# Optimization experiments

Hardware: AMD Instinct MI355X
Metric: run time of the kernel (lower is better)

The kernel has to match this reference:

```python
import jax, jax.numpy as jnp
import numpy as np

BETA = 30.0


def setup_inputs() -> dict:
    key = jax.random.key(0)
    k_x, k1, k2, k3, kv = jax.random.split(key, 5)
    B, D = 4096, 128
    N = 32  # nodes per hidden layer
    VALUE_SCALE = 500.0
    return {
        "x": jax.random.normal(k_x, (B, D), dtype=jnp.float32),
        "W1": jax.random.normal(k1, (N, D), dtype=jnp.float32),
        "W2": jax.random.normal(k2, (N, D), dtype=jnp.float32),
        "W3": jax.random.normal(k3, (N, D), dtype=jnp.float32),
        "V": jax.random.normal(kv, (1, N, N, N), dtype=jnp.float32) / VALUE_SCALE,
    }


def reference(x, W1, W2, W3, V):
    # feat='sf': every gating layer reads the raw input x (h is never updated).
    # gate_i = sigmoid(beta * x @ W_i^T), shape [B, 32]
    g1 = jax.nn.sigmoid(BETA * (x @ W1.T))
    g2 = jax.nn.sigmoid(BETA * (x @ W2.T))
    g3 = jax.nn.sigmoid(BETA * (x @ W3.T))
    # prod='op': cp[b,i,j,k] = g1[b,i]*g2[b,j]*g3[b,k];
    # out[b] = sum_{ijk} cp[b,i,j,k] * V[0,i,j,k]  -- expressed as one contraction.
    return jnp.einsum("bi,bj,bk,ijk->b", g1, g2, g3, V[0])
```

## Files before the change

kernel.cpp:

```cpp
#include <hip/hip_runtime.h>


#define BETA 30.0f

__device__ __forceinline__ float f4c(const float4 v, int c) {
    return c == 0 ? v.x : (c == 1 ? v.y : (c == 2 ? v.z : v.w));
}

__global__ __launch_bounds__(256, 2) void dlgn_v11_kernel(
    const float* __restrict__ x,
    const float* __restrict__ W1,
    const float* __restrict__ W2,
    const float* __restrict__ W3,
    const float* __restrict__ V,
    float* __restrict__ out)
{
    __shared__ float xlds[8 * 160];
    __shared__ float Gs[8][100];
    __shared__ float red[4][8];

    const int t  = threadIdx.x;
    const int b0 = blockIdx.x * 8;

    {
        const int r    = t >> 5;
        const int col4 = t & 31;
        const float4 xv = ((const float4*)(x + (size_t)(b0 + r) * 128))[col4];
        const int skc = col4 >> 2, sc = col4 & 3;
        *(float4*)&xlds[r * 160 + skc * 20 + sc * 4] = xv;
    }

    const int fl = t >> 3;
    const int kc = t & 7;
    float4 w1c[4], w2c[4], w3c[4];
    {
        const float4* W1r = (const float4*)(W1 + fl * 128 + kc * 16);
        const float4* W2r = (const float4*)(W2 + fl * 128 + kc * 16);
        const float4* W3r = (const float4*)(W3 + fl * 128 + kc * 16);
#pragma unroll
        for (int c = 0; c < 4; ++c) {
            w1c[c] = W1r[c]; w2c[c] = W2r[c]; w3c[c] = W3r[c];
        }
    }
    __syncthreads();

    float acc[3][8];
#pragma unroll
    for (int m = 0; m < 3; ++m)
#pragma unroll
        for (int r = 0; r < 8; ++r) acc[m][r] = 0.f;

#pragma unroll
    for (int r = 0; r < 8; ++r) {
        float4 xc[4];
#pragma unroll
        for (int c = 0; c < 4; ++c)
            xc[c] = *(const float4*)&xlds[r * 160 + kc * 20 + c * 4];
#pragma unroll
        for (int c = 0; c < 4; ++c) {
            acc[0][r] = fmaf(w1c[c].x, xc[c].x, acc[0][r]);
            acc[0][r] = fmaf(w1c[c].y, xc[c].y, acc[0][r]);
            acc[0][r] = fmaf(w1c[c].z, xc[c].z, acc[0][r]);
            acc[0][r] = fmaf(w1c[c].w, xc[c].w, acc[0][r]);
            acc[1][r] = fmaf(w2c[c].x, xc[c].x, acc[1][r]);
            acc[1][r] = fmaf(w2c[c].y, xc[c].y, acc[1][r]);
            acc[1][r] = fmaf(w2c[c].z, xc[c].z, acc[1][r]);
            acc[1][r] = fmaf(w2c[c].w, xc[c].w, acc[1][r]);
            acc[2][r] = fmaf(w3c[c].x, xc[c].x, acc[2][r]);
            acc[2][r] = fmaf(w3c[c].y, xc[c].y, acc[2][r]);
            acc[2][r] = fmaf(w3c[c].z, xc[c].z, acc[2][r]);
            acc[2][r] = fmaf(w3c[c].w, xc[c].w, acc[2][r]);
        }
    }

    const float4* V4 = (const float4*)V;
    float4 v[32];
#pragma unroll
    for (int i = 0; i < 32; ++i) v[i] = V4[i * 256 + t];

#pragma unroll
    for (int m = 0; m < 3; ++m) {
        float sel = 0.f;
#pragma unroll
        for (int r = 0; r < 8; ++r) {
            float a = acc[m][r];
            a += __shfl_xor(a, 1);
            a += __shfl_xor(a, 2);
            a += __shfl_xor(a, 4);
            if (kc == r) sel = a;
        }
        Gs[kc][32 * m + fl] = 1.0f / (1.0f + __expf(-BETA * sel));
    }
    __syncthreads();

    const int j  = t >> 3;
    const int c2 = t & 7;
    const int w  = t >> 6;
    const int l  = t & 63;

    for (int b = 0; b < 8; ++b) {
        const float4* Gr = (const float4*)&Gs[b][0];
        float4 g1r[8];
#pragma unroll
        for (int c = 0; c < 8; ++c) g1r[c] = Gr[c];
        const float4 g3r = *(const float4*)&Gs[b][64 + c2 * 4];
        const float  g2s = Gs[b][32 + j];

        float ux = 0.f, uy = 0.f, uz = 0.f, uw = 0.f;
#pragma unroll
        for (int i = 0; i < 32; ++i) {
            const float g1i = f4c(g1r[i >> 2], i & 3);
            ux = fmaf(g1i, v[i].x, ux);
            uy = fmaf(g1i, v[i].y, uy);
            uz = fmaf(g1i, v[i].z, uz);
            uw = fmaf(g1i, v[i].w, uw);
        }
        float s = ux * g3r.x;
        s = fmaf(uy, g3r.y, s);
        s = fmaf(uz, g3r.z, s);
        s = fmaf(uw, g3r.w, s);
        float p = s * g2s;

        p += __shfl_xor(p, 1);
        p += __shfl_xor(p, 2);
        p += __shfl_xor(p, 4);
        p += __shfl_xor(p, 8);
        p += __shfl_xor(p, 16);
        p += __shfl_xor(p, 32);
        if (l == 0) red[w][b] = p;
    }
    __syncthreads();

    if (t < 8) out[b0 + t] = red[0][t] + red[1][t] + red[2][t] + red[3][t];
}

extern "C" void kernel_launch(void* const* d_in, const int* in_sizes, int n_in,
                              void* d_out, int out_size, void* d_ws, size_t ws_size,
                              hipStream_t stream) {
    const float* x  = (const float*)d_in[0];
    const float* W1 = (const float*)d_in[1];
    const float* W2 = (const float*)d_in[2];
    const float* W3 = (const float*)d_in[3];
    const float* V  = (const float*)d_in[4];
    float* out = (float*)d_out;

    dlgn_v11_kernel<<<dim3(512), dim3(256), 0, stream>>>(x, W1, W2, W3, V, out);
}
```

Measured before the change: 15.20 us.

## Use DPP and readlane broadcasts and defer cross-thread reduction to one LDS pass

Replaces the first two xor shuffles in the gate reduction with DPP quad-permute moves. The inner contraction now gets g1 values by broadcasting them with readlane instead of reloading eight float4s from LDS for each batch row. The eight per-row wave reductions, each six shuffles long, become a single LDS transpose followed by one reduction pass. This removes LDS traffic and shuffle latency inside the hot loop, at the cost of a larger LDS buffer and a different summation order.

```diff
diff --git a/kernel.cpp b/kernel.cpp
--- a/kernel.cpp
+++ b/kernel.cpp
@@ -7,7 +7,14 @@
     return c == 0 ? v.x : (c == 1 ? v.y : (c == 2 ? v.z : v.w));
 }
 
-__global__ __launch_bounds__(256, 2) void dlgn_v11_kernel(
+__device__ __forceinline__ float qp_xor1(float a) {
+    return __int_as_float(__builtin_amdgcn_mov_dpp(__float_as_int(a), 0xB1, 0xF, 0xF, true));
+}
+__device__ __forceinline__ float qp_xor2(float a) {
+    return __int_as_float(__builtin_amdgcn_mov_dpp(__float_as_int(a), 0x4E, 0xF, 0xF, true));
+}
+
+__global__ __launch_bounds__(256, 2) void dlgn_v12_kernel(
     const float* __restrict__ x,
     const float* __restrict__ W1,
     const float* __restrict__ W2,
@@ -17,7 +24,7 @@
 {
     __shared__ float xlds[8 * 160];
     __shared__ float Gs[8][100];
-    __shared__ float red[4][8];
+    __shared__ float Plds[2560];
 
     const int t  = threadIdx.x;
     const int b0 = blockIdx.x * 8;
@@ -84,8 +91,8 @@
 #pragma unroll
         for (int r = 0; r < 8; ++r) {
             float a = acc[m][r];
-            a += __shfl_xor(a, 1);
-            a += __shfl_xor(a, 2);
+            a += qp_xor1(a);
+            a += qp_xor2(a);
             a += __shfl_xor(a, 4);
             if (kc == r) sel = a;
         }
@@ -95,21 +102,19 @@
 
     const int j  = t >> 3;
     const int c2 = t & 7;
-    const int w  = t >> 6;
-    const int l  = t & 63;
 
+    float p8[8];
+#pragma unroll
     for (int b = 0; b < 8; ++b) {
-        const float4* Gr = (const float4*)&Gs[b][0];
-        float4 g1r[8];
-#pragma unroll
-        for (int c = 0; c < 8; ++c) g1r[c] = Gr[c];
+        const float  ga  = Gs[b][t & 31];
+        const float  g2s = Gs[b][32 + j];
         const float4 g3r = *(const float4*)&Gs[b][64 + c2 * 4];
-        const float  g2s = Gs[b][32 + j];
 
         float ux = 0.f, uy = 0.f, uz = 0.f, uw = 0.f;
 #pragma unroll
         for (int i = 0; i < 32; ++i) {
-            const float g1i = f4c(g1r[i >> 2], i & 3);
+            const float g1i = __int_as_float(
+                __builtin_amdgcn_readlane(__float_as_int(ga), i));
             ux = fmaf(g1i, v[i].x, ux);
             uy = fmaf(g1i, v[i].y, uy);
             uz = fmaf(g1i, v[i].z, uz);
@@ -119,19 +124,27 @@
         s = fmaf(uy, g3r.y, s);
         s = fmaf(uz, g3r.z, s);
         s = fmaf(uw, g3r.w, s);
-        float p = s * g2s;
+        p8[b] = s * g2s;
+    }
 
-        p += __shfl_xor(p, 1);
-        p += __shfl_xor(p, 2);
-        p += __shfl_xor(p, 4);
-        p += __shfl_xor(p, 8);
-        p += __shfl_xor(p, 16);
-        p += __shfl_xor(p, 32);
-        if (l == 0) red[w][b] = p;
-    }
+    *(float4*)&Plds[t * 10]     = make_float4(p8[0], p8[1], p8[2], p8[3]);
+    *(float4*)&Plds[t * 10 + 4] = make_float4(p8[4], p8[5], p8[6], p8[7]);
     __syncthreads();
 
-    if (t < 8) out[b0 + t] = red[0][t] + red[1][t] + red[2][t] + red[3][t];
+    {
+        const int fb2 = t >> 5;
+        const int pt  = t & 31;
+        float s = 0.f;
+#pragma unroll
+        for (int s8 = 0; s8 < 8; ++s8)
+            s += Plds[(pt + s8 * 32) * 10 + fb2];
+        s += __shfl_xor(s, 1);
+        s += __shfl_xor(s, 2);
+        s += __shfl_xor(s, 4);
+        s += __shfl_xor(s, 8);
+        s += __shfl_xor(s, 16);
+        if (pt == 0) out[b0 + fb2] = s;
+    }
 }
 
 extern "C" void kernel_launch(void* const* d_in, const int* in_sizes, int n_in,
@@ -144,5 +157,5 @@
     const float* V  = (const float*)d_in[4];
     float* out = (float*)d_out;
 
-    dlgn_v11_kernel<<<dim3(512), dim3(256), 0, stream>>>(x, W1, W2, W3, V, out);
+    dlgn_v12_kernel<<<dim3(512), dim3(256), 0, stream>>>(x, W1, W2, W3, V, out);
 }
```

Measured after the change: 13.97 us. -8.1%, faster.
